# Kernel tuning notes

Measured on AMD Instinct MI355X. Metric: run time of the kernel, lower is better.

## Reference

```python
import jax, jax.numpy as jnp
import numpy as np

N_NODES = 50000


def _gcn_conv(x, src, dst, norm, W, b):
    # x: [N, F_in], src/dst: [E+N] (self loops included), norm: [E+N]
    h = x @ W                                   # [N, F_out]
    msg = h[src] * norm[:, None]                # [E+N, F_out] gather + scale
    out = jax.ops.segment_sum(msg, dst, num_segments=N_NODES)  # scatter-add
    return out + b


def _norm_coeffs(edge_index, n_nodes):
    # PyG GCNConv: add self loops, deg over dst (col), norm = d^-1/2[src]*d^-1/2[dst]
    loops = jnp.arange(n_nodes, dtype=edge_index.dtype)
    src = jnp.concatenate([edge_index[0], loops])
    dst = jnp.concatenate([edge_index[1], loops])
    deg = jax.ops.segment_sum(jnp.ones_like(dst, dtype=jnp.float32), dst,
                              num_segments=n_nodes)
    dinv = jnp.where(deg > 0, jax.lax.rsqrt(jnp.maximum(deg, 1.0)), 0.0)
    norm = dinv[src] * dinv[dst]
    return src, dst, norm


def setup_inputs() -> dict:
    key = jax.random.key(0)
    ks = jax.random.split(key, 8)
    F_in, F_hid, E = 128, 128, 600000
    x = jax.random.normal(ks[0], (N_NODES, F_in), dtype=jnp.float32)
    edge_index = jax.random.randint(ks[1], (2, E), 0, N_NODES, dtype=jnp.int32)
    s1 = 1.0 / np.sqrt(F_in)
    s2 = 1.0 / np.sqrt(F_hid)
    W1 = jax.random.uniform(ks[2], (F_in, F_hid), jnp.float32, -s1, s1)
    b1 = jnp.zeros((F_hid,), jnp.float32)
    W2 = jax.random.uniform(ks[3], (F_hid, F_hid), jnp.float32, -s2, s2)
    b2 = jnp.zeros((F_hid,), jnp.float32)
    W3 = jax.random.uniform(ks[4], (F_hid, F_hid), jnp.float32, -s2, s2)
    b3 = jnp.zeros((F_hid,), jnp.float32)
    return {"x": x, "edge_index": edge_index,
            "W1": W1, "b1": b1, "W2": W2, "b2": b2, "W3": W3, "b3": b3}


def reference(x, edge_index, W1, b1, W2, b2, W3, b3):
    src, dst, norm = _norm_coeffs(edge_index, N_NODES)
    h = jax.nn.relu(_gcn_conv(x, src, dst, norm, W1, b1))
    h = jax.nn.relu(_gcn_conv(h, src, dst, norm, W2, b2))
    h = _gcn_conv(h, src, dst, norm, W3, b3)
    # original forward returns (x, h) with x rebound to h (identical arrays)
    return (h, h)
```

## Files before the change

kernel.cpp:

```cpp
#include <hip/hip_runtime.h>

#define NNODES 50000
#define FDIM 128
#define KELL 40

typedef float f4 __attribute__((ext_vector_type(4)));
typedef float f2 __attribute__((ext_vector_type(2)));
typedef short short8 __attribute__((ext_vector_type(8)));
typedef uint uint4v __attribute__((ext_vector_type(4)));
typedef uint uint2v __attribute__((ext_vector_type(2)));

__device__ __forceinline__ void split2(float x0, float x1, unsigned& hi, unsigned& lo) {
    unsigned u0 = __float_as_uint(x0), u1 = __float_as_uint(x1);
    unsigned h0 = u0 & 0xffff0000u, h1 = u1 & 0xffff0000u;
    hi = h1 | (h0 >> 16);
    float l0 = x0 - __uint_as_float(h0);
    float l1 = x1 - __uint_as_float(h1);
    lo = (__float_as_uint(l1) & 0xffff0000u) | (__float_as_uint(l0) >> 16);
}

__device__ __forceinline__ unsigned pack2(float lo, float hi) {
    unsigned ul = __float_as_uint(lo);
    unsigned uh = __float_as_uint(hi);
    ul += 0x7fffu + ((ul >> 16) & 1u);
    uh += 0x7fffu + ((uh >> 16) & 1u);
    return (ul >> 16) | (uh & 0xffff0000u);
}

__device__ __forceinline__ f4 dec(uint2v v) {
    f4 r;
    r.x = __uint_as_float(v.x << 16);
    r.y = __uint_as_float(v.x & 0xffff0000u);
    r.z = __uint_as_float(v.y << 16);
    r.w = __uint_as_float(v.y & 0xffff0000u);
    return r;
}

__device__ __forceinline__ void prepw_body(const float* __restrict__ W,
                                           unsigned* __restrict__ dh, int p) {
    unsigned* dl = dh + 8192;
    int jp = p & 3;
    int l = (p >> 2) & 63;
    int st = p >> 8;
    int s = st >> 3, t = st & 7;
    int k0 = ((l >> 4) << 3) + (jp << 1) + (s << 5);
    int n = (t << 4) + (l & 15);
    float x0 = W[k0 * 128 + n];
    float x1 = W[(k0 + 1) * 128 + n];
    unsigned hi, lo;
    split2(x0, x1, hi, lo);
    dh[p] = hi;
    dl[p] = lo;
}

#define NB_PREP 96
#define NB_ZERO 196

__global__ __launch_bounds__(256) void k_pre(const float* __restrict__ W1,
                                             const float* __restrict__ W2,
                                             const float* __restrict__ W3,
                                             unsigned* __restrict__ wpk,
                                             int* __restrict__ fill) {
    int bid = blockIdx.x;
    int tid = threadIdx.x;
    if (bid < NB_PREP) {
        int y = bid >> 5;
        const float* W = (y == 0) ? W1 : (y == 1) ? W2 : W3;
        prepw_body(W, wpk + (size_t)y * 16384, (bid & 31) * 256 + tid);
    } else {
        int i = (bid - NB_PREP) * 256 + tid;
        if (i < NNODES) fill[i] = 0;
    }
}

__device__ __forceinline__ void fill_body(const int* __restrict__ src,
                                          const int* __restrict__ dst,
                                          int* __restrict__ fill,
                                          int* __restrict__ col, int E, int i) {
    int e0 = i * 2;
    if (e0 + 1 < E) {
        int2 s2 = *(const int2*)(src + e0);
        int2 d2 = *(const int2*)(dst + e0);
        int slot0 = atomicAdd(&fill[d2.x], 1);
        int slot1 = atomicAdd(&fill[d2.y], 1);
        if (slot0 < KELL) col[d2.x * KELL + slot0] = s2.x;
        if (slot1 < KELL) col[d2.y * KELL + slot1] = s2.y;
    } else if (e0 < E) {
        int d = dst[e0];
        int slot = atomicAdd(&fill[d], 1);
        if (slot < KELL) col[d * KELL + slot] = src[e0];
    }
}

__device__ __forceinline__ void gemm1_body(const float* __restrict__ A,
                                           const unsigned* __restrict__ wsrc,
                                           unsigned* __restrict__ H, int nrows,
                                           int bid, int tid) {
    int w = tid >> 6, l = tid & 63;
    int m16 = l & 15, q = l >> 4;
    int rbase = bid * 64 + w * 16;
    int row = rbase + m16;
    int rowc = row > nrows - 1 ? nrows - 1 : row;

    union u8 { unsigned u[4]; uint4v uv; short8 v; };
    u8 ah[4], al[4];
    const f4* A4 = (const f4*)A;
#pragma unroll
    for (int s = 0; s < 4; ++s) {
        f4 a0 = A4[(size_t)rowc * 32 + s * 8 + q * 2];
        f4 a1 = A4[(size_t)rowc * 32 + s * 8 + q * 2 + 1];
        split2(a0.x, a0.y, ah[s].u[0], al[s].u[0]);
        split2(a0.z, a0.w, ah[s].u[1], al[s].u[1]);
        split2(a1.x, a1.y, ah[s].u[2], al[s].u[2]);
        split2(a1.z, a1.w, ah[s].u[3], al[s].u[3]);
    }

    f4 acc[8];
#pragma unroll
    for (int t = 0; t < 8; ++t) acc[t] = (f4)0.0f;

    const uint4v* wg4 = (const uint4v*)wsrc;
#pragma unroll
    for (int s = 0; s < 4; ++s) {
#pragma unroll
        for (int t = 0; t < 8; ++t) {
            u8 bh, bl;
            bh.uv = wg4[(s * 8 + t) * 64 + l];
            bl.uv = wg4[2048 + (s * 8 + t) * 64 + l];
            acc[t] = __builtin_amdgcn_mfma_f32_16x16x32_bf16(ah[s].v, bh.v, acc[t], 0, 0, 0);
            acc[t] = __builtin_amdgcn_mfma_f32_16x16x32_bf16(al[s].v, bh.v, acc[t], 0, 0, 0);
            acc[t] = __builtin_amdgcn_mfma_f32_16x16x32_bf16(ah[s].v, bl.v, acc[t], 0, 0, 0);
        }
    }

#pragma unroll
    for (int up = 0; up < 4; ++up) {
#pragma unroll
        for (int r = 0; r < 4; ++r) {
            int rr = rbase + q * 4 + r;
            if (rr < nrows)
                H[(size_t)rr * 64 + up * 16 + m16] =
                    pack2(acc[2 * up][r], acc[2 * up + 1][r]);
        }
    }
}

__global__ __launch_bounds__(256, 4) void k_fillgemm(const float* __restrict__ x,
                                                     const int* __restrict__ src,
                                                     const int* __restrict__ dst,
                                                     int* __restrict__ fill,
                                                     int* __restrict__ col, int E, int gb,
                                                     const unsigned* __restrict__ wpk,
                                                     unsigned* __restrict__ H) {
    int bid = blockIdx.x;
    int tid = threadIdx.x;
    if (bid < gb) {
        gemm1_body(x, wpk, H, NNODES, bid, tid);
    } else {
        fill_body(src, dst, fill, col, E, (bid - gb) * 256 + tid);
    }
}

__global__ __launch_bounds__(128, 5) void k_fused(const unsigned* __restrict__ hin,
                                                  const int* __restrict__ fill,
                                                  const int* __restrict__ col,
                                                  const float* __restrict__ bias,
                                                  const unsigned* __restrict__ wsrc,
                                                  unsigned* __restrict__ hout) {
    __shared__ float As[16][132];
    int tid = threadIdx.x;
    int w = tid >> 6, l = tid & 63;
    int half = l >> 5;
    int sl = l & 31;
    int hb = half * 32;
    int nbase = blockIdx.x * 16;

    const uint2v* h2 = (const uint2v*)hin;
#pragma unroll 1
    for (int it = 0; it < 4; ++it) {
        int rl = w * 8 + it * 2 + half;
        int n = nbase + rl;
        int deg = fill[n];
        int c = deg < KELL ? deg : KELL;
        float di = rsqrtf(1.0f + (float)deg);
        f4 a = di * dec(h2[(size_t)n * 32 + sl]);

        int beg = n * KELL;
        int cv = 0;
        float wv = 0.0f;
        if (sl < c) {
            cv = col[beg + sl];
            wv = rsqrtf(1.0f + (float)fill[cv]);
        }
        int j = 0;
#pragma unroll 1
        for (; j + 8 <= c; j += 8) {
            int s0 = __shfl(cv, hb + j);
            int s1 = __shfl(cv, hb + j + 1);
            int s2 = __shfl(cv, hb + j + 2);
            int s3 = __shfl(cv, hb + j + 3);
            int s4 = __shfl(cv, hb + j + 4);
            int s5 = __shfl(cv, hb + j + 5);
            int s6 = __shfl(cv, hb + j + 6);
            int s7 = __shfl(cv, hb + j + 7);
            float w0 = __shfl(wv, hb + j);
            float w1 = __shfl(wv, hb + j + 1);
            float w2 = __shfl(wv, hb + j + 2);
            float w3 = __shfl(wv, hb + j + 3);
            float w4 = __shfl(wv, hb + j + 4);
            float w5 = __shfl(wv, hb + j + 5);
            float w6 = __shfl(wv, hb + j + 6);
            float w7 = __shfl(wv, hb + j + 7);
            uint2v v0 = h2[(size_t)s0 * 32 + sl];
            uint2v v1 = h2[(size_t)s1 * 32 + sl];
            uint2v v2 = h2[(size_t)s2 * 32 + sl];
            uint2v v3 = h2[(size_t)s3 * 32 + sl];
            uint2v v4 = h2[(size_t)s4 * 32 + sl];
            uint2v v5 = h2[(size_t)s5 * 32 + sl];
            uint2v v6 = h2[(size_t)s6 * 32 + sl];
            uint2v v7 = h2[(size_t)s7 * 32 + sl];
            a += w0 * dec(v0); a += w1 * dec(v1); a += w2 * dec(v2); a += w3 * dec(v3);
            a += w4 * dec(v4); a += w5 * dec(v5); a += w6 * dec(v6); a += w7 * dec(v7);
        }
#pragma unroll 1
        for (; j + 4 <= c; j += 4) {
            int s0 = __shfl(cv, hb + j);
            int s1 = __shfl(cv, hb + j + 1);
            int s2 = __shfl(cv, hb + j + 2);
            int s3 = __shfl(cv, hb + j + 3);
            float w0 = __shfl(wv, hb + j);
            float w1 = __shfl(wv, hb + j + 1);
            float w2 = __shfl(wv, hb + j + 2);
            float w3 = __shfl(wv, hb + j + 3);
            uint2v v0 = h2[(size_t)s0 * 32 + sl];
            uint2v v1 = h2[(size_t)s1 * 32 + sl];
            uint2v v2 = h2[(size_t)s2 * 32 + sl];
            uint2v v3 = h2[(size_t)s3 * 32 + sl];
            a += w0 * dec(v0); a += w1 * dec(v1); a += w2 * dec(v2); a += w3 * dec(v3);
        }
#pragma unroll 1
        for (; j < c; ++j) {
            int s = __shfl(cv, hb + j);
            float wgt = __shfl(wv, hb + j);
            a += wgt * dec(h2[(size_t)s * 32 + sl]);
        }

        int u = sl >> 3;
        int m = (sl & 7) * 2;
        int c0 = u * 32 + m;
        f2 b0 = *(const f2*)(bias + c0);
        f2 b1v = *(const f2*)(bias + c0 + 16);
        f2 o0, o1;
        o0.x = fmaxf(di * a.x + b0.x, 0.0f);
        o0.y = fmaxf(di * a.z + b0.y, 0.0f);
        o1.x = fmaxf(di * a.y + b1v.x, 0.0f);
        o1.y = fmaxf(di * a.w + b1v.y, 0.0f);
        *(f2*)&As[rl][c0] = o0;
        *(f2*)&As[rl][c0 + 16] = o1;
    }
    __syncthreads();

    int m16 = l & 15, q = l >> 4;
    union u8 { unsigned u[4]; uint4v uv; short8 v; };
    u8 ah[4], al[4];
#pragma unroll
    for (int s = 0; s < 4; ++s) {
        f4 a0 = *(const f4*)&As[m16][s * 32 + q * 8];
        f4 a1 = *(const f4*)&As[m16][s * 32 + q * 8 + 4];
        split2(a0.x, a0.y, ah[s].u[0], al[s].u[0]);
        split2(a0.z, a0.w, ah[s].u[1], al[s].u[1]);
        split2(a1.x, a1.y, ah[s].u[2], al[s].u[2]);
        split2(a1.z, a1.w, ah[s].u[3], al[s].u[3]);
    }

    f4 acc[4];
#pragma unroll
    for (int tt = 0; tt < 4; ++tt) acc[tt] = (f4)0.0f;

    const uint4v* wg4 = (const uint4v*)wsrc;
#pragma unroll
    for (int s = 0; s < 4; ++s) {
#pragma unroll
        for (int tt = 0; tt < 4; ++tt) {
            int t = w * 4 + tt;
            u8 bh, bl;
            bh.uv = wg4[(s * 8 + t) * 64 + l];
            bl.uv = wg4[2048 + (s * 8 + t) * 64 + l];
            acc[tt] = __builtin_amdgcn_mfma_f32_16x16x32_bf16(ah[s].v, bh.v, acc[tt], 0, 0, 0);
            acc[tt] = __builtin_amdgcn_mfma_f32_16x16x32_bf16(al[s].v, bh.v, acc[tt], 0, 0, 0);
            acc[tt] = __builtin_amdgcn_mfma_f32_16x16x32_bf16(ah[s].v, bl.v, acc[tt], 0, 0, 0);
        }
    }

#pragma unroll
    for (int p = 0; p < 2; ++p) {
#pragma unroll
        for (int r = 0; r < 4; ++r) {
            int rr = nbase + q * 4 + r;
            hout[(size_t)rr * 64 + (2 * w + p) * 16 + m16] =
                pack2(acc[2 * p][r], acc[2 * p + 1][r]);
        }
    }
}

__global__ __launch_bounds__(256) void k_agg(const unsigned* __restrict__ hpk,
                                             const int* __restrict__ fill,
                                             const int* __restrict__ col,
                                             const float* __restrict__ bias,
                                             float* __restrict__ out,
                                             float* __restrict__ out2) {
    int gw = (blockIdx.x * 256 + threadIdx.x) >> 6;
    int lane = threadIdx.x & 63;
    int half = lane >> 5;
    int sl = lane & 31;
    int hb = half * 32;
    int n = gw * 2 + half;
    if (n >= NNODES) return;
    int deg = fill[n];
    int c = deg < KELL ? deg : KELL;
    float di = rsqrtf(1.0f + (float)deg);

    const uint2v* h2 = (const uint2v*)hpk;
    f4 a = di * dec(h2[(size_t)n * 32 + sl]);

    int beg = n * KELL;
    {
        int cv = 0;
        float wv = 0.0f;
        if (sl < c) {
            cv = col[beg + sl];
            wv = rsqrtf(1.0f + (float)fill[cv]);
        }
        int j = 0;
#pragma unroll 1
        for (; j + 8 <= c; j += 8) {
            int s0 = __shfl(cv, hb + j);
            int s1 = __shfl(cv, hb + j + 1);
            int s2 = __shfl(cv, hb + j + 2);
            int s3 = __shfl(cv, hb + j + 3);
            int s4 = __shfl(cv, hb + j + 4);
            int s5 = __shfl(cv, hb + j + 5);
            int s6 = __shfl(cv, hb + j + 6);
            int s7 = __shfl(cv, hb + j + 7);
            float w0 = __shfl(wv, hb + j);
            float w1 = __shfl(wv, hb + j + 1);
            float w2 = __shfl(wv, hb + j + 2);
            float w3 = __shfl(wv, hb + j + 3);
            float w4 = __shfl(wv, hb + j + 4);
            float w5 = __shfl(wv, hb + j + 5);
            float w6 = __shfl(wv, hb + j + 6);
            float w7 = __shfl(wv, hb + j + 7);
            uint2v v0 = h2[(size_t)s0 * 32 + sl];
            uint2v v1 = h2[(size_t)s1 * 32 + sl];
            uint2v v2 = h2[(size_t)s2 * 32 + sl];
            uint2v v3 = h2[(size_t)s3 * 32 + sl];
            uint2v v4 = h2[(size_t)s4 * 32 + sl];
            uint2v v5 = h2[(size_t)s5 * 32 + sl];
            uint2v v6 = h2[(size_t)s6 * 32 + sl];
            uint2v v7 = h2[(size_t)s7 * 32 + sl];
            a += w0 * dec(v0); a += w1 * dec(v1); a += w2 * dec(v2); a += w3 * dec(v3);
            a += w4 * dec(v4); a += w5 * dec(v5); a += w6 * dec(v6); a += w7 * dec(v7);
        }
#pragma unroll 1
        for (; j + 4 <= c; j += 4) {
            int s0 = __shfl(cv, hb + j);
            int s1 = __shfl(cv, hb + j + 1);
            int s2 = __shfl(cv, hb + j + 2);
            int s3 = __shfl(cv, hb + j + 3);
            float w0 = __shfl(wv, hb + j);
            float w1 = __shfl(wv, hb + j + 1);
            float w2 = __shfl(wv, hb + j + 2);
            float w3 = __shfl(wv, hb + j + 3);
            uint2v v0 = h2[(size_t)s0 * 32 + sl];
            uint2v v1 = h2[(size_t)s1 * 32 + sl];
            uint2v v2 = h2[(size_t)s2 * 32 + sl];
            uint2v v3 = h2[(size_t)s3 * 32 + sl];
            a += w0 * dec(v0); a += w1 * dec(v1); a += w2 * dec(v2); a += w3 * dec(v3);
        }
#pragma unroll 1
        for (; j < c; ++j) {
            int s = __shfl(cv, hb + j);
            float wgt = __shfl(wv, hb + j);
            a += wgt * dec(h2[(size_t)s * 32 + sl]);
        }
    }

    int u = sl >> 3;
    int m = (sl & 7) * 2;
    int c0 = u * 32 + m;
    f2 b0 = *(const f2*)(bias + c0);
    f2 b1 = *(const f2*)(bias + c0 + 16);
    f2 o0, o1;
    o0.x = di * a.x + b0.x;
    o0.y = di * a.z + b0.y;
    o1.x = di * a.y + b1.x;
    o1.y = di * a.w + b1.y;
    float* orow = out + (size_t)n * FDIM;
    *(f2*)(orow + c0) = o0;
    *(f2*)(orow + c0 + 16) = o1;
    float* orow2 = out2 + (size_t)n * FDIM;
    *(f2*)(orow2 + c0) = o0;
    *(f2*)(orow2 + c0 + 16) = o1;
}

extern "C" void kernel_launch(void* const* d_in, const int* in_sizes, int n_in,
                              void* d_out, int out_size, void* d_ws, size_t ws_size,
                              hipStream_t stream) {
    const float* x  = (const float*)d_in[0];
    const int*   ei = (const int*)d_in[1];
    const float* W1 = (const float*)d_in[2];
    const float* b1 = (const float*)d_in[3];
    const float* W2 = (const float*)d_in[4];
    const float* b2 = (const float*)d_in[5];
    const float* W3 = (const float*)d_in[6];
    const float* b3 = (const float*)d_in[7];
    int E = in_sizes[1] / 2;
    const int* srcp = ei;
    const int* dstp = ei + E;
    float* outf = (float*)d_out;

    unsigned* hpkA = (unsigned*)d_ws;
    int*      fill = (int*)(hpkA + (size_t)NNODES * 64);
    int*      col  = fill + NNODES;
    unsigned* wpk  = (unsigned*)(col + (size_t)NNODES * KELL);
    unsigned* hpkB = (unsigned*)outf;

    int eb = (E / 2 + 255) / 256;
    int gb = (NNODES + 63) / 64;
    int fb = NNODES / 16;
    int ab = (NNODES / 2 * 64 + 255) / 256;

    k_pre<<<NB_PREP + NB_ZERO, 256, 0, stream>>>(W1, W2, W3, wpk, fill);
    k_fillgemm<<<gb + eb, 256, 0, stream>>>(x, srcp, dstp, fill, col, E, gb,
                                            wpk, hpkA);
    k_fused<<<fb, 128, 0, stream>>>(hpkA, fill, col, b1, wpk + 16384, hpkB);
    k_fused<<<fb, 128, 0, stream>>>(hpkB, fill, col, b2, wpk + 32768, hpkA);
    k_agg<<<ab, 256, 0, stream>>>(hpkA, fill, col, b3, outf,
                                  outf + (size_t)NNODES * FDIM);
}
```

Before: 220.6 us.

## Gather rows with 16 lanes and 16-byte loads, shrink ELL columns to ushort

Each node's aggregation now uses a 16-lane group that loads 16 bytes per lane (uint4) instead of 32 lanes with 8-byte loads, so a wave handles four nodes at once. Neighbours are consumed in chunks of 16 so the shuffle source stays within the group. ELL column indices are stored as 16-bit unsigned shorts, which halves the index traffic and relies on node ids fitting in 16 bits (50000 < 65536). The fill kernel now processes one edge per thread. The occupancy hint on k_fused drops from 5 to 4, and the extra chunk loop adds some overhead.

After: 225.8 us. +2.4%, slower.

```diff
diff --git a/kernel.cpp b/kernel.cpp
--- a/kernel.cpp
+++ b/kernel.cpp
@@ -8,7 +8,7 @@
 typedef float f2 __attribute__((ext_vector_type(2)));
 typedef short short8 __attribute__((ext_vector_type(8)));
 typedef uint uint4v __attribute__((ext_vector_type(4)));
-typedef uint uint2v __attribute__((ext_vector_type(2)));
+typedef unsigned short ushortt;
 
 __device__ __forceinline__ void split2(float x0, float x1, unsigned& hi, unsigned& lo) {
     unsigned u0 = __float_as_uint(x0), u1 = __float_as_uint(x1);
@@ -27,12 +27,20 @@
     return (ul >> 16) | (uh & 0xffff0000u);
 }
 
-__device__ __forceinline__ f4 dec(uint2v v) {
+__device__ __forceinline__ f4 dlo(uint4v v) {
     f4 r;
     r.x = __uint_as_float(v.x << 16);
-    r.y = __uint_as_float(v.x & 0xffff0000u);
-    r.z = __uint_as_float(v.y << 16);
-    r.w = __uint_as_float(v.y & 0xffff0000u);
+    r.y = __uint_as_float(v.y << 16);
+    r.z = __uint_as_float(v.z << 16);
+    r.w = __uint_as_float(v.w << 16);
+    return r;
+}
+__device__ __forceinline__ f4 dhi(uint4v v) {
+    f4 r;
+    r.x = __uint_as_float(v.x & 0xffff0000u);
+    r.y = __uint_as_float(v.y & 0xffff0000u);
+    r.z = __uint_as_float(v.z & 0xffff0000u);
+    r.w = __uint_as_float(v.w & 0xffff0000u);
     return r;
 }
 
@@ -76,20 +84,12 @@
 __device__ __forceinline__ void fill_body(const int* __restrict__ src,
                                           const int* __restrict__ dst,
                                           int* __restrict__ fill,
-                                          int* __restrict__ col, int E, int i) {
-    int e0 = i * 2;
-    if (e0 + 1 < E) {
-        int2 s2 = *(const int2*)(src + e0);
-        int2 d2 = *(const int2*)(dst + e0);
-        int slot0 = atomicAdd(&fill[d2.x], 1);
-        int slot1 = atomicAdd(&fill[d2.y], 1);
-        if (slot0 < KELL) col[d2.x * KELL + slot0] = s2.x;
-        if (slot1 < KELL) col[d2.y * KELL + slot1] = s2.y;
-    } else if (e0 < E) {
-        int d = dst[e0];
-        int slot = atomicAdd(&fill[d], 1);
-        if (slot < KELL) col[d * KELL + slot] = src[e0];
-    }
+                                          ushortt* __restrict__ col, int E, int i) {
+    if (i >= E) return;
+    int d = dst[i];
+    int s = src[i];
+    int slot = atomicAdd(&fill[d], 1);
+    if (slot < KELL) col[d * KELL + slot] = (ushortt)s;
 }
 
 __device__ __forceinline__ void gemm1_body(const float* __restrict__ A,
@@ -149,7 +149,8 @@
                                                      const int* __restrict__ src,
                                                      const int* __restrict__ dst,
                                                      int* __restrict__ fill,
-                                                     int* __restrict__ col, int E, int gb,
+                                                     ushortt* __restrict__ col,
+                                                     int E, int gb,
                                                      const unsigned* __restrict__ wpk,
                                                      unsigned* __restrict__ H) {
     int bid = blockIdx.x;
@@ -161,102 +162,128 @@
     }
 }
 
-__global__ __launch_bounds__(128, 5) void k_fused(const unsigned* __restrict__ hin,
+__device__ __forceinline__ void gather16(const unsigned* __restrict__ hpk,
+                                         const int* __restrict__ fillv,
+                                         const ushortt* __restrict__ colu,
+                                         const float* __restrict__ bias,
+                                         int n, int sl, int gb16,
+                                         f4& olo, f4& ohi) {
+    int deg = fillv[n];
+    int c = deg < KELL ? deg : KELL;
+    float di = rsqrtf(1.0f + (float)deg);
+    const uint4v* h4 = (const uint4v*)hpk;
+    uint4v sq = h4[(size_t)n * 16 + sl];
+    f4 alo = di * dlo(sq);
+    f4 ahi = di * dhi(sq);
+    int beg = n * KELL;
+#pragma unroll 1
+    for (int b = 0; b < c; b += 16) {
+        int cb = c - b;
+        if (cb > 16) cb = 16;
+        int cv = 0;
+        float wv = 0.0f;
+        if (sl < cb) {
+            cv = colu[beg + b + sl];
+            wv = rsqrtf(1.0f + (float)fillv[cv]);
+        }
+        int j = 0;
+#pragma unroll 1
+        for (; j + 8 <= cb; j += 8) {
+            int s0 = __shfl(cv, gb16 + j);
+            int s1 = __shfl(cv, gb16 + j + 1);
+            int s2 = __shfl(cv, gb16 + j + 2);
+            int s3 = __shfl(cv, gb16 + j + 3);
+            int s4 = __shfl(cv, gb16 + j + 4);
+            int s5 = __shfl(cv, gb16 + j + 5);
+            int s6 = __shfl(cv, gb16 + j + 6);
+            int s7 = __shfl(cv, gb16 + j + 7);
+            float w0 = __shfl(wv, gb16 + j);
+            float w1 = __shfl(wv, gb16 + j + 1);
+            float w2 = __shfl(wv, gb16 + j + 2);
+            float w3 = __shfl(wv, gb16 + j + 3);
+            float w4 = __shfl(wv, gb16 + j + 4);
+            float w5 = __shfl(wv, gb16 + j + 5);
+            float w6 = __shfl(wv, gb16 + j + 6);
+            float w7 = __shfl(wv, gb16 + j + 7);
+            uint4v v0 = h4[(size_t)s0 * 16 + sl];
+            uint4v v1 = h4[(size_t)s1 * 16 + sl];
+            uint4v v2 = h4[(size_t)s2 * 16 + sl];
+            uint4v v3 = h4[(size_t)s3 * 16 + sl];
+            uint4v v4 = h4[(size_t)s4 * 16 + sl];
+            uint4v v5 = h4[(size_t)s5 * 16 + sl];
+            uint4v v6 = h4[(size_t)s6 * 16 + sl];
+            uint4v v7 = h4[(size_t)s7 * 16 + sl];
+            alo += w0 * dlo(v0); ahi += w0 * dhi(v0);
+            alo += w1 * dlo(v1); ahi += w1 * dhi(v1);
+            alo += w2 * dlo(v2); ahi += w2 * dhi(v2);
+            alo += w3 * dlo(v3); ahi += w3 * dhi(v3);
+            alo += w4 * dlo(v4); ahi += w4 * dhi(v4);
+            alo += w5 * dlo(v5); ahi += w5 * dhi(v5);
+            alo += w6 * dlo(v6); ahi += w6 * dhi(v6);
+            alo += w7 * dlo(v7); ahi += w7 * dhi(v7);
+        }
+#pragma unroll 1
+        for (; j + 4 <= cb; j += 4) {
+            int s0 = __shfl(cv, gb16 + j);
+            int s1 = __shfl(cv, gb16 + j + 1);
+            int s2 = __shfl(cv, gb16 + j + 2);
+            int s3 = __shfl(cv, gb16 + j + 3);
+            float w0 = __shfl(wv, gb16 + j);
+            float w1 = __shfl(wv, gb16 + j + 1);
+            float w2 = __shfl(wv, gb16 + j + 2);
+            float w3 = __shfl(wv, gb16 + j + 3);
+            uint4v v0 = h4[(size_t)s0 * 16 + sl];
+            uint4v v1 = h4[(size_t)s1 * 16 + sl];
+            uint4v v2 = h4[(size_t)s2 * 16 + sl];
+            uint4v v3 = h4[(size_t)s3 * 16 + sl];
+            alo += w0 * dlo(v0); ahi += w0 * dhi(v0);
+            alo += w1 * dlo(v1); ahi += w1 * dhi(v1);
+            alo += w2 * dlo(v2); ahi += w2 * dhi(v2);
+            alo += w3 * dlo(v3); ahi += w3 * dhi(v3);
+        }
+#pragma unroll 1
+        for (; j < cb; ++j) {
+            int s = __shfl(cv, gb16 + j);
+            float wgt = __shfl(wv, gb16 + j);
+            uint4v v = h4[(size_t)s * 16 + sl];
+            alo += wgt * dlo(v);
+            ahi += wgt * dhi(v);
+        }
+    }
+    int u = sl >> 2;
+    int c0 = u * 32 + (sl & 3) * 4;
+    f4 blo = *(const f4*)(bias + c0);
+    f4 bhi = *(const f4*)(bias + c0 + 16);
+    olo = di * alo + blo;
+    ohi = di * ahi + bhi;
+}
+
+__global__ __launch_bounds__(128, 4) void k_fused(const unsigned* __restrict__ hin,
                                                   const int* __restrict__ fill,
-                                                  const int* __restrict__ col,
+                                                  const ushortt* __restrict__ colu,
                                                   const float* __restrict__ bias,
                                                   const unsigned* __restrict__ wsrc,
                                                   unsigned* __restrict__ hout) {
     __shared__ float As[16][132];
     int tid = threadIdx.x;
     int w = tid >> 6, l = tid & 63;
-    int half = l >> 5;
-    int sl = l & 31;
-    int hb = half * 32;
+    int g = l >> 4, sl = l & 15, gb16 = g * 16;
     int nbase = blockIdx.x * 16;
-
-    const uint2v* h2 = (const uint2v*)hin;
-#pragma unroll 1
-    for (int it = 0; it < 4; ++it) {
-        int rl = w * 8 + it * 2 + half;
+    int u = sl >> 2;
+    int c0 = u * 32 + (sl & 3) * 4;
+
+#pragma unroll 1
+    for (int it = 0; it < 2; ++it) {
+        int rl = w * 8 + it * 4 + g;
         int n = nbase + rl;
-        int deg = fill[n];
-        int c = deg < KELL ? deg : KELL;
-        float di = rsqrtf(1.0f + (float)deg);
-        f4 a = di * dec(h2[(size_t)n * 32 + sl]);
-
-        int beg = n * KELL;
-        int cv = 0;
-        float wv = 0.0f;
-        if (sl < c) {
-            cv = col[beg + sl];
-            wv = rsqrtf(1.0f + (float)fill[cv]);
-        }
-        int j = 0;
-#pragma unroll 1
-        for (; j + 8 <= c; j += 8) {
-            int s0 = __shfl(cv, hb + j);
-            int s1 = __shfl(cv, hb + j + 1);
-            int s2 = __shfl(cv, hb + j + 2);
-            int s3 = __shfl(cv, hb + j + 3);
-            int s4 = __shfl(cv, hb + j + 4);
-            int s5 = __shfl(cv, hb + j + 5);
-            int s6 = __shfl(cv, hb + j + 6);
-            int s7 = __shfl(cv, hb + j + 7);
-            float w0 = __shfl(wv, hb + j);
-            float w1 = __shfl(wv, hb + j + 1);
-            float w2 = __shfl(wv, hb + j + 2);
-            float w3 = __shfl(wv, hb + j + 3);
-            float w4 = __shfl(wv, hb + j + 4);
-            float w5 = __shfl(wv, hb + j + 5);
-            float w6 = __shfl(wv, hb + j + 6);
-            float w7 = __shfl(wv, hb + j + 7);
-            uint2v v0 = h2[(size_t)s0 * 32 + sl];
-            uint2v v1 = h2[(size_t)s1 * 32 + sl];
-            uint2v v2 = h2[(size_t)s2 * 32 + sl];
-            uint2v v3 = h2[(size_t)s3 * 32 + sl];
-            uint2v v4 = h2[(size_t)s4 * 32 + sl];
-            uint2v v5 = h2[(size_t)s5 * 32 + sl];
-            uint2v v6 = h2[(size_t)s6 * 32 + sl];
-            uint2v v7 = h2[(size_t)s7 * 32 + sl];
-            a += w0 * dec(v0); a += w1 * dec(v1); a += w2 * dec(v2); a += w3 * dec(v3);
-            a += w4 * dec(v4); a += w5 * dec(v5); a += w6 * dec(v6); a += w7 * dec(v7);
-        }
-#pragma unroll 1
-        for (; j + 4 <= c; j += 4) {
-            int s0 = __shfl(cv, hb + j);
-            int s1 = __shfl(cv, hb + j + 1);
-            int s2 = __shfl(cv, hb + j + 2);
-            int s3 = __shfl(cv, hb + j + 3);
-            float w0 = __shfl(wv, hb + j);
-            float w1 = __shfl(wv, hb + j + 1);
-            float w2 = __shfl(wv, hb + j + 2);
-            float w3 = __shfl(wv, hb + j + 3);
-            uint2v v0 = h2[(size_t)s0 * 32 + sl];
-            uint2v v1 = h2[(size_t)s1 * 32 + sl];
-            uint2v v2 = h2[(size_t)s2 * 32 + sl];
-            uint2v v3 = h2[(size_t)s3 * 32 + sl];
-            a += w0 * dec(v0); a += w1 * dec(v1); a += w2 * dec(v2); a += w3 * dec(v3);
-        }
-#pragma unroll 1
-        for (; j < c; ++j) {
-            int s = __shfl(cv, hb + j);
-            float wgt = __shfl(wv, hb + j);
-            a += wgt * dec(h2[(size_t)s * 32 + sl]);
-        }
-
-        int u = sl >> 3;
-        int m = (sl & 7) * 2;
-        int c0 = u * 32 + m;
-        f2 b0 = *(const f2*)(bias + c0);
-        f2 b1v = *(const f2*)(bias + c0 + 16);
-        f2 o0, o1;
-        o0.x = fmaxf(di * a.x + b0.x, 0.0f);
-        o0.y = fmaxf(di * a.z + b0.y, 0.0f);
-        o1.x = fmaxf(di * a.y + b1v.x, 0.0f);
-        o1.y = fmaxf(di * a.w + b1v.y, 0.0f);
-        *(f2*)&As[rl][c0] = o0;
-        *(f2*)&As[rl][c0 + 16] = o1;
+        f4 olo, ohi;
+        gather16(hin, fill, colu, bias, n, sl, gb16, olo, ohi);
+        olo.x = fmaxf(olo.x, 0.0f); olo.y = fmaxf(olo.y, 0.0f);
+        olo.z = fmaxf(olo.z, 0.0f); olo.w = fmaxf(olo.w, 0.0f);
+        ohi.x = fmaxf(ohi.x, 0.0f); ohi.y = fmaxf(ohi.y, 0.0f);
+        ohi.z = fmaxf(ohi.z, 0.0f); ohi.w = fmaxf(ohi.w, 0.0f);
+        *(f4*)&As[rl][c0] = olo;
+        *(f4*)&As[rl][c0 + 16] = ohi;
     }
     __syncthreads();
 
@@ -303,104 +330,28 @@
     }
 }
 
-__global__ __launch_bounds__(256) void k_agg(const unsigned* __restrict__ hpk,
-                                             const int* __restrict__ fill,
-                                             const int* __restrict__ col,
-                                             const float* __restrict__ bias,
-                                             float* __restrict__ out,
-                                             float* __restrict__ out2) {
+__global__ __launch_bounds__(256, 4) void k_agg(const unsigned* __restrict__ hpk,
+                                                const int* __restrict__ fill,
+                                                const ushortt* __restrict__ colu,
+                                                const float* __restrict__ bias,
+                                                float* __restrict__ out,
+                                                float* __restrict__ out2) {
     int gw = (blockIdx.x * 256 + threadIdx.x) >> 6;
-    int lane = threadIdx.x & 63;
-    int half = lane >> 5;
-    int sl = lane & 31;
-    int hb = half * 32;
-    int n = gw * 2 + half;
-    if (n >= NNODES) return;
-    int deg = fill[n];
-    int c = deg < KELL ? deg : KELL;
-    float di = rsqrtf(1.0f + (float)deg);
-
-    const uint2v* h2 = (const uint2v*)hpk;
-    f4 a = di * dec(h2[(size_t)n * 32 + sl]);
-
-    int beg = n * KELL;
-    {
-        int cv = 0;
-        float wv = 0.0f;
-        if (sl < c) {
-            cv = col[beg + sl];
-            wv = rsqrtf(1.0f + (float)fill[cv]);
-        }
-        int j = 0;
-#pragma unroll 1
-        for (; j + 8 <= c; j += 8) {
-            int s0 = __shfl(cv, hb + j);
-            int s1 = __shfl(cv, hb + j + 1);
-            int s2 = __shfl(cv, hb + j + 2);
-            int s3 = __shfl(cv, hb + j + 3);
-            int s4 = __shfl(cv, hb + j + 4);
-            int s5 = __shfl(cv, hb + j + 5);
-            int s6 = __shfl(cv, hb + j + 6);
-            int s7 = __shfl(cv, hb + j + 7);
-            float w0 = __shfl(wv, hb + j);
-            float w1 = __shfl(wv, hb + j + 1);
-            float w2 = __shfl(wv, hb + j + 2);
-            float w3 = __shfl(wv, hb + j + 3);
-            float w4 = __shfl(wv, hb + j + 4);
-            float w5 = __shfl(wv, hb + j + 5);
-            float w6 = __shfl(wv, hb + j + 6);
-            float w7 = __shfl(wv, hb + j + 7);
-            uint2v v0 = h2[(size_t)s0 * 32 + sl];
-            uint2v v1 = h2[(size_t)s1 * 32 + sl];
-            uint2v v2 = h2[(size_t)s2 * 32 + sl];
-            uint2v v3 = h2[(size_t)s3 * 32 + sl];
-            uint2v v4 = h2[(size_t)s4 * 32 + sl];
-            uint2v v5 = h2[(size_t)s5 * 32 + sl];
-            uint2v v6 = h2[(size_t)s6 * 32 + sl];
-            uint2v v7 = h2[(size_t)s7 * 32 + sl];
-            a += w0 * dec(v0); a += w1 * dec(v1); a += w2 * dec(v2); a += w3 * dec(v3);
-            a += w4 * dec(v4); a += w5 * dec(v5); a += w6 * dec(v6); a += w7 * dec(v7);
-        }
-#pragma unroll 1
-        for (; j + 4 <= c; j += 4) {
-            int s0 = __shfl(cv, hb + j);
-            int s1 = __shfl(cv, hb + j + 1);
-            int s2 = __shfl(cv, hb + j + 2);
-            int s3 = __shfl(cv, hb + j + 3);
-            float w0 = __shfl(wv, hb + j);
-            float w1 = __shfl(wv, hb + j + 1);
-            float w2 = __shfl(wv, hb + j + 2);
-            float w3 = __shfl(wv, hb + j + 3);
-            uint2v v0 = h2[(size_t)s0 * 32 + sl];
-            uint2v v1 = h2[(size_t)s1 * 32 + sl];
-            uint2v v2 = h2[(size_t)s2 * 32 + sl];
-            uint2v v3 = h2[(size_t)s3 * 32 + sl];
-            a += w0 * dec(v0); a += w1 * dec(v1); a += w2 * dec(v2); a += w3 * dec(v3);
-        }
-#pragma unroll 1
-        for (; j < c; ++j) {
-            int s = __shfl(cv, hb + j);
-            float wgt = __shfl(wv, hb + j);
-            a += wgt * dec(h2[(size_t)s * 32 + sl]);
-        }
-    }
-
-    int u = sl >> 3;
-    int m = (sl & 7) * 2;
-    int c0 = u * 32 + m;
-    f2 b0 = *(const f2*)(bias + c0);
-    f2 b1 = *(const f2*)(bias + c0 + 16);
-    f2 o0, o1;
-    o0.x = di * a.x + b0.x;
-    o0.y = di * a.z + b0.y;
-    o1.x = di * a.y + b1.x;
-    o1.y = di * a.w + b1.y;
+    int l = threadIdx.x & 63;
+    int g = l >> 4, sl = l & 15, gb16 = g * 16;
+    int n = gw * 4 + g;
+
+    f4 olo, ohi;
+    gather16(hpk, fill, colu, bias, n, sl, gb16, olo, ohi);
+
+    int u = sl >> 2;
+    int c0 = u * 32 + (sl & 3) * 4;
     float* orow = out + (size_t)n * FDIM;
-    *(f2*)(orow + c0) = o0;
-    *(f2*)(orow + c0 + 16) = o1;
+    *(f4*)(orow + c0) = olo;
+    *(f4*)(orow + c0 + 16) = ohi;
     float* orow2 = out2 + (size_t)n * FDIM;
-    *(f2*)(orow2 + c0) = o0;
-    *(f2*)(orow2 + c0 + 16) = o1;
+    *(f4*)(orow2 + c0) = olo;
+    *(f4*)(orow2 + c0 + 16) = ohi;
 }
 
 extern "C" void kernel_launch(void* const* d_in, const int* in_sizes, int n_in,
@@ -421,20 +372,20 @@
 
     unsigned* hpkA = (unsigned*)d_ws;
     int*      fill = (int*)(hpkA + (size_t)NNODES * 64);
-    int*      col  = fill + NNODES;
-    unsigned* wpk  = (unsigned*)(col + (size_t)NNODES * KELL);
+    ushortt*  colu = (ushortt*)(fill + NNODES);
+    unsigned* wpk  = (unsigned*)(colu + (size_t)NNODES * KELL);
     unsigned* hpkB = (unsigned*)outf;
 
-    int eb = (E / 2 + 255) / 256;
+    int eb = (E + 255) / 256;
     int gb = (NNODES + 63) / 64;
     int fb = NNODES / 16;
-    int ab = (NNODES / 2 * 64 + 255) / 256;
+    int ab = NNODES / 16;
 
     k_pre<<<NB_PREP + NB_ZERO, 256, 0, stream>>>(W1, W2, W3, wpk, fill);
-    k_fillgemm<<<gb + eb, 256, 0, stream>>>(x, srcp, dstp, fill, col, E, gb,
+    k_fillgemm<<<gb + eb, 256, 0, stream>>>(x, srcp, dstp, fill, colu, E, gb,
                                             wpk, hpkA);
-    k_fused<<<fb, 128, 0, stream>>>(hpkA, fill, col, b1, wpk + 16384, hpkB);
-    k_fused<<<fb, 128, 0, stream>>>(hpkB, fill, col, b2, wpk + 32768, hpkA);
-    k_agg<<<ab, 256, 0, stream>>>(hpkA, fill, col, b3, outf,
+    k_fused<<<fb, 128, 0, stream>>>(hpkA, fill, colu, b1, wpk + 16384, hpkB);
+    k_fused<<<fb, 128, 0, stream>>>(hpkB, fill, colu, b2, wpk + 32768, hpkA);
+    k_agg<<<ab, 256, 0, stream>>>(hpkA, fill, colu, b3, outf,
                                   outf + (size_t)NNODES * FDIM);
 }
```
